# Kernel optimization log

Measured on AMD Instinct MI355X. Metric: run time of the kernel, lower is better.

Reference implementation:

```python
import jax, jax.numpy as jnp
import numpy as np

B, S, D, H = 2, 2048, 1024, 16
DK = D // H
NEG = -1.0e9

def setup_inputs() -> dict:
    key = jax.random.key(0)
    ks = jax.random.split(key, 12)
    sc = 1.0 / np.sqrt(D)
    q = jax.random.normal(ks[0], (B, S, D), jnp.float32)
    k = jax.random.normal(ks[1], (B, S, D), jnp.float32)
    v = jax.random.normal(ks[2], (B, S, D), jnp.float32)
    # causal mask: True = masked (matches masked_fill(mask == True, -1e9))
    mask = jnp.broadcast_to(jnp.triu(jnp.ones((S, S), bool), k=1)[None, None], (B, 1, S, S))
    Wq = jax.random.normal(ks[3], (D, D), jnp.float32) * sc
    bq = jnp.zeros((D,), jnp.float32)
    Wk = jax.random.normal(ks[4], (D, D), jnp.float32) * sc
    bk = jnp.zeros((D,), jnp.float32)
    Wv = jax.random.normal(ks[5], (D, D), jnp.float32) * sc
    bv = jnp.zeros((D,), jnp.float32)
    Wo = jax.random.normal(ks[6], (D, D), jnp.float32) * sc
    bo = jnp.zeros((D,), jnp.float32)
    return {"q": q, "k": k, "v": v, "mask": mask,
            "Wq": Wq, "bq": bq, "Wk": Wk, "bk": bk,
            "Wv": Wv, "bv": bv, "Wo": Wo, "bo": bo}

def reference(q, k, v, mask, Wq, bq, Wk, bk, Wv, bv, Wo, bo):
    def split_heads(x):  # [B,S,D] -> [B,H,S,DK]
        return x.reshape(B, S, H, DK).transpose(0, 2, 1, 3)
    qh = split_heads(q @ Wq + bq)
    kh = split_heads(k @ Wk + bk)
    vh = split_heads(v @ Wv + bv)
    scores = jnp.einsum('bhqd,bhkd->bhqk', qh, kh) / np.sqrt(DK)
    scores = jnp.where(mask, NEG, scores)
    p = jax.nn.softmax(scores, axis=-1)
    out = jnp.einsum('bhqk,bhkd->bhqd', p, vh)  # [B,H,S,DK]
    out = out.transpose(0, 2, 1, 3).reshape(B, S, D)
    return out @ Wo + bo
```

## Files before the change

kernel.cpp:

```cpp
#include <hip/hip_runtime.h>

#define BB 2
#define SS 2048
#define DD 1024
#define HH 16
#define DKK 64

typedef __attribute__((ext_vector_type(8))) short short8;
typedef __attribute__((ext_vector_type(4))) float floatx4;

__device__ inline float bf2f(ushort u) {
    union { unsigned int i; float f; } x; x.i = ((unsigned int)u) << 16; return x.f;
}
__device__ inline ushort f2bf(float f) {
    union { float f; unsigned int i; } x; x.f = f;
    unsigned int r = x.i + 0x7fff + ((x.i >> 16) & 1);
    return (ushort)(r >> 16);
}
__device__ inline void async_cp16(const ushort* g, ushort* l) {
    __builtin_amdgcn_global_load_lds(
        (const __attribute__((address_space(1))) unsigned int*)g,
        (__attribute__((address_space(3))) unsigned int*)l, 16, 0, 0);
}
__device__ inline unsigned int cvt_pk_bf16(float lo, float hi) {
    unsigned int r;
    asm("v_cvt_pk_bf16_f32 %0, %1, %2" : "=v"(r) : "v"(lo), "v"(hi));
    return r;
}
__device__ inline void swap32(unsigned int& a, unsigned int& b) {
    asm("v_permlane32_swap_b32 %0, %1" : "+v"(a), "+v"(b));
}
__device__ inline void swap16(unsigned int& a, unsigned int& b) {
    asm("v_permlane16_swap_b32 %0, %1" : "+v"(a), "+v"(b));
}

__global__ __launch_bounds__(256) void cvt_all(const float* __restrict__ q,
                                               const float* __restrict__ k,
                                               const float* __restrict__ v,
                                               const float* __restrict__ w0,
                                               const float* __restrict__ w1,
                                               const float* __restrict__ w2,
                                               const float* __restrict__ w3,
                                               ushort* __restrict__ oq,
                                               ushort* __restrict__ ok,
                                               ushort* __restrict__ ov,
                                               ushort* __restrict__ t0,
                                               ushort* __restrict__ t1,
                                               ushort* __restrict__ t2,
                                               ushort* __restrict__ t3) {
    __shared__ ushort t[32][33];
    int z = blockIdx.z;
    if (z < 3) {
        const float* in = (z == 0) ? q : (z == 1) ? k : v;
        ushort* out = (z == 0) ? oq : (z == 1) ? ok : ov;
        int i = blockIdx.x * 256 + threadIdx.x;
        float4 f0 = ((const float4*)in)[i * 2];
        float4 f1 = ((const float4*)in)[i * 2 + 1];
        short8 p;
        p[0] = (short)f2bf(f0.x); p[1] = (short)f2bf(f0.y);
        p[2] = (short)f2bf(f0.z); p[3] = (short)f2bf(f0.w);
        p[4] = (short)f2bf(f1.x); p[5] = (short)f2bf(f1.y);
        p[6] = (short)f2bf(f1.z); p[7] = (short)f2bf(f1.w);
        ((short8*)out)[i] = p;
    } else {
        int m = (z - 3) * 2 + (blockIdx.x >> 10);
        int tile = blockIdx.x & 1023;
        int bx = tile & 31, by = tile >> 5;
        const float* in = (m == 0) ? w0 : (m == 1) ? w1 : (m == 2) ? w2 : w3;
        ushort* out = (m == 0) ? t0 : (m == 1) ? t1 : (m == 2) ? t2 : t3;
        int tx = threadIdx.x & 31, ty = threadIdx.x >> 5;
        for (int i = ty; i < 32; i += 8)
            t[i][tx] = f2bf(in[(size_t)(by * 32 + i) * DD + bx * 32 + tx]);
        __syncthreads();
        for (int i = ty; i < 32; i += 8)
            out[(size_t)(bx * 32 + i) * DD + by * 32 + tx] = t[tx][i];
    }
}

__global__ __launch_bounds__(256, 3) void gemm_qkv(const ushort* __restrict__ Xq,
                                                   const ushort* __restrict__ Xk,
                                                   const ushort* __restrict__ Xv,
                                                   const ushort* __restrict__ WtQ,
                                                   const ushort* __restrict__ WtK,
                                                   const ushort* __restrict__ WtV,
                                                   const float* __restrict__ bq,
                                                   const float* __restrict__ bk,
                                                   const float* __restrict__ bv,
                                                   ushort* __restrict__ qh,
                                                   ushort* __restrict__ kh,
                                                   ushort* __restrict__ vt) {
    constexpr int K = 1024;
    constexpr int NKT = 32;
    __shared__ ushort smem[16384];

    int lin = blockIdx.x + ((blockIdx.y + (blockIdx.z << 5)) << 3);
    int wid = (lin & 7) * 96 + (lin >> 3);
    int z = wid >> 8;
    int rem = wid & 255;
    int byy = rem >> 3, bxx = rem & 7;
    int rowBase = byy * 128, colBase = bxx * 128;

    const ushort* Ag = (z == 0) ? Xq : (z == 1) ? Xk : Xv;
    const ushort* Bg = (z == 0) ? WtQ : (z == 1) ? WtK : WtV;
    const float* bias = (z == 0) ? bq : (z == 1) ? bk : bv;
    ushort* outp = (z == 0) ? qh : (z == 1) ? kh : vt;

    int tid = threadIdx.x;
    int wave = tid >> 6, lane = tid & 63, quad = lane >> 4, l15 = lane & 15;
    int wm = wave >> 1, wn = wave & 1;

    size_t srcA[2], srcB[2];
    int dstU[2];
#pragma unroll
    for (int r = 0; r < 2; ++r) {
        int lb = r * 4096 + wave * 1024 + lane * 16;
        int sl = lb ^ (((lb >> 9) & 1) << 5);
        int srow = sl >> 6;
        int scol = (sl & 63) >> 1;
        srcA[r] = (size_t)(rowBase + srow) * K + scol;
        srcB[r] = (size_t)(colBase + srow) * K + scol;
        dstU[r] = r * 2048 + wave * 512;
    }
    int aOff[4], bOff[4];
#pragma unroll
    for (int mi = 0; mi < 4; ++mi) {
        int row = wm * 64 + mi * 16 + l15;
        aOff[mi] = row * 32 + ((quad * 8) ^ (((row >> 3) & 1) << 4));
    }
#pragma unroll
    for (int ni = 0; ni < 4; ++ni) {
        int row = wn * 64 + ni * 16 + l15;
        bOff[ni] = 4096 + row * 32 + ((quad * 8) ^ (((row >> 3) & 1) << 4));
    }

    auto stageTile = [&](int u) {
        int slot = (u & 1) << 13;
        const ushort* As = Ag + u * 32;
        const ushort* Bs = Bg + u * 32;
        async_cp16(As + srcA[0], &smem[slot + dstU[0]]);
        async_cp16(As + srcA[1], &smem[slot + dstU[1]]);
        async_cp16(Bs + srcB[0], &smem[slot + 4096 + dstU[0]]);
        async_cp16(Bs + srcB[1], &smem[slot + 4096 + dstU[1]]);
    };

    floatx4 acc[4][4] = {};
    stageTile(0);
    for (int t = 0; t < NKT; ++t) {
        if (t < NKT - 1) {
            stageTile(t + 1);
            asm volatile("s_waitcnt vmcnt(4)" ::: "memory");
        } else {
            asm volatile("s_waitcnt vmcnt(0)" ::: "memory");
        }
        __builtin_amdgcn_s_barrier();
        __builtin_amdgcn_sched_barrier(0);
        int slot = (t & 1) << 13;
        short8 bfr[4], af[4];
#pragma unroll
        for (int ni = 0; ni < 4; ++ni)
            bfr[ni] = *(const short8*)&smem[slot + bOff[ni]];
#pragma unroll
        for (int mi = 0; mi < 4; ++mi)
            af[mi] = *(const short8*)&smem[slot + aOff[mi]];
#pragma unroll
        for (int mi = 0; mi < 4; ++mi)
#pragma unroll
            for (int ni = 0; ni < 4; ++ni)
                acc[mi][ni] = __builtin_amdgcn_mfma_f32_16x16x32_bf16(
                    af[mi], bfr[ni], acc[mi][ni], 0, 0, 0);
        __builtin_amdgcn_sched_barrier(0);
        __builtin_amdgcn_s_barrier();
    }

    float bvv[4];
#pragma unroll
    for (int ni = 0; ni < 4; ++ni)
        bvv[ni] = bias[colBase + wn * 64 + ni * 16 + l15];
    if (z == 2) {
#pragma unroll
        for (int mi = 0; mi < 4; ++mi)
#pragma unroll
            for (int ni = 0; ni < 4; ++ni) {
                int col = colBase + wn * 64 + ni * 16 + l15;
                int h = col >> 6, dk = col & 63;
                int rowg = rowBase + wm * 64 + mi * 16 + quad * 4;
                int b = rowg >> 11, s = rowg & 2047;
                int2 v;
                v.x = (int)cvt_pk_bf16(acc[mi][ni][0] + bvv[ni], acc[mi][ni][1] + bvv[ni]);
                v.y = (int)cvt_pk_bf16(acc[mi][ni][2] + bvv[ni], acc[mi][ni][3] + bvv[ni]);
                *(int2*)&outp[((size_t)((b * HH + h) * DKK + dk)) * SS + s] = v;
            }
    } else {
#pragma unroll
        for (int mi = 0; mi < 4; ++mi)
#pragma unroll
            for (int ni = 0; ni < 4; ++ni) {
                int col = colBase + wn * 64 + ni * 16 + l15;
                int h = col >> 6, dk = col & 63;
#pragma unroll
                for (int i = 0; i < 4; ++i) {
                    int rowg = rowBase + wm * 64 + mi * 16 + quad * 4 + i;
                    int b = rowg >> 11, s = rowg & 2047;
                    outp[((size_t)((b * HH + h) * SS + s)) * DKK + dk] =
                        f2bf(acc[mi][ni][i] + bvv[ni]);
                }
            }
    }
}

__global__ __launch_bounds__(256) void gemm_fin(const ushort* __restrict__ A,
                                                const ushort* __restrict__ Bt,
                                                const float* __restrict__ bias,
                                                float* __restrict__ outp) {
    constexpr int K = 1024, N = 1024, NT = 32;
    __shared__ ushort smem[12288];
    int tid = threadIdx.x;
    int wave = tid >> 6, lane = tid & 63, quad = lane >> 4, l15 = lane & 15;
    int wm = wave >> 1, wn = wave & 1;

    int lin = blockIdx.x + (blockIdx.y << 3);
    int wid = (lin & 7) * 64 + (lin >> 3);
    int bx = wid & 7, by = wid >> 3;
    int rowBase = by * 64, colBase = bx * 128;

    auto stage = [&](int k0, int d) {
        int ab = d * 6144, bb2 = 2048 + d * 6144;
#pragma unroll
        for (int j = 0; j < 3; ++j) {
            int c = j * 4 + wave;
            int cbase = (c < 4) ? c * 64 : (c - 4) * 64;
            int cc = cbase + lane;
            int row = cc >> 2, sub = (cc & 3) * 8;
            if (c < 4)
                async_cp16(&A[(size_t)(rowBase + row) * K + k0 + sub], &smem[ab + cbase * 8]);
            else
                async_cp16(&Bt[(size_t)(colBase + row) * K + k0 + sub], &smem[bb2 + cbase * 8]);
        }
    };

    floatx4 acc[2][4] = {};
    stage(0, 0);
    __syncthreads();
    for (int t = 0; t < NT; ++t) {
        if (t + 1 < NT) stage((t + 1) * 32, (t + 1) & 1);
        int ab = (t & 1) * 6144, bb2 = 2048 + (t & 1) * 6144;
        short8 af[2], bf[4];
#pragma unroll
        for (int mi = 0; mi < 2; ++mi)
            af[mi] = *(const short8*)&smem[ab + (wm * 32 + mi * 16 + l15) * 32 + quad * 8];
#pragma unroll
        for (int ni = 0; ni < 4; ++ni)
            bf[ni] = *(const short8*)&smem[bb2 + (wn * 64 + ni * 16 + l15) * 32 + quad * 8];
#pragma unroll
        for (int mi = 0; mi < 2; ++mi)
#pragma unroll
            for (int ni = 0; ni < 4; ++ni)
                acc[mi][ni] = __builtin_amdgcn_mfma_f32_16x16x32_bf16(
                    af[mi], bf[ni], acc[mi][ni], 0, 0, 0);
        __syncthreads();
    }
    for (int mi = 0; mi < 2; ++mi)
        for (int ni = 0; ni < 4; ++ni) {
            int col = colBase + wn * 64 + ni * 16 + l15;
            float bv = bias[col];
            for (int i = 0; i < 4; ++i) {
                int row = rowBase + wm * 32 + mi * 16 + quad * 4 + i;
                outp[(size_t)row * N + col] = acc[mi][ni][i] + bv;
            }
        }
}

__global__ __launch_bounds__(256, 2) void flash_attn5(const ushort* __restrict__ qh,
                                                      const ushort* __restrict__ kh,
                                                      const ushort* __restrict__ vt,
                                                      ushort* __restrict__ attn) {
    constexpr int LD = 72;
    __shared__ ushort Ksm[2][64 * LD];
    __shared__ ushort Vsm[2][64 * LD];
    int tid = threadIdx.x;
    int wave = tid >> 6, lane = tid & 63, quad = lane >> 4, l15 = lane & 15;

    int lin = blockIdx.x + (blockIdx.y << 4) + (blockIdx.z << 8);
    int wid = (lin & 7) * 64 + (lin >> 3);
    const int qt0 = wid & 15;
    int h = (wid >> 4) & 15;
    int b = wid >> 8;
    const int qt1 = 31 - qt0;

    const size_t headQK = ((size_t)(b * HH + h)) * SS * DKK;
    const size_t headV  = ((size_t)(b * HH + h)) * DKK * SS;
    int c0 = tid, r0 = c0 >> 3, s0 = (c0 & 7) * 8;
    int c1 = tid + 256, r1 = c1 >> 3, s1 = (c1 & 7) * 8;

    int qrow0 = qt0 * 64 + wave * 16 + l15;
    int qrow1 = qt1 * 64 + wave * 16 + l15;
    short8 q0a = *(const short8*)&qh[headQK + (size_t)qrow0 * DKK + quad * 8];
    short8 q0b = *(const short8*)&qh[headQK + (size_t)qrow0 * DKK + 32 + quad * 8];
    short8 q1a = *(const short8*)&qh[headQK + (size_t)qrow1 * DKK + quad * 8];
    short8 q1b = *(const short8*)&qh[headQK + (size_t)qrow1 * DKK + 32 + quad * 8];

    floatx4 o0[4] = {}, o1[4] = {};
    float l0 = 0.f, l1 = 0.f;
    int qsel = wave * 16 + l15;

    *(int4*)&Ksm[0][r0 * LD + s0] = *(const int4*)&kh[headQK + (size_t)r0 * DKK + s0];
    *(int4*)&Ksm[0][r1 * LD + s1] = *(const int4*)&kh[headQK + (size_t)r1 * DKK + s1];
    *(int4*)&Vsm[0][r0 * LD + s0] = *(const int4*)&vt[headV + (size_t)r0 * SS + s0];
    *(int4*)&Vsm[0][r1 * LD + s1] = *(const int4*)&vt[headV + (size_t)r1 * SS + s1];
    __syncthreads();

    for (int kt = 0; kt <= qt1; ++kt) {
        int cur = kt & 1;
        bool pre = (kt < qt1);
        bool act0 = (kt <= qt0);
        int4 kA, kB, vA, vB;
        if (pre) {
            const ushort* kp = &kh[headQK + (size_t)((kt + 1) * 64) * DKK];
            const ushort* vp = &vt[headV + (kt + 1) * 64];
            kA = *(const int4*)&kp[(size_t)r0 * DKK + s0];
            kB = *(const int4*)&kp[(size_t)r1 * DKK + s1];
            vA = *(const int4*)&vp[(size_t)r0 * SS + s0];
            vB = *(const int4*)&vp[(size_t)r1 * SS + s1];
        }
        floatx4 sv1[4], sv0[4];
        __builtin_amdgcn_s_setprio(1);
#pragma unroll
        for (int cn = 0; cn < 4; ++cn) {
            short8 kf0 = *(const short8*)&Ksm[cur][(cn * 16 + l15) * LD + quad * 8];
            short8 kf1 = *(const short8*)&Ksm[cur][(cn * 16 + l15) * LD + 32 + quad * 8];
            floatx4 zz = {};
            zz = __builtin_amdgcn_mfma_f32_16x16x32_bf16(kf0, q1a, zz, 0, 0, 0);
            zz = __builtin_amdgcn_mfma_f32_16x16x32_bf16(kf1, q1b, zz, 0, 0, 0);
            sv1[cn] = zz;
            if (act0) {
                floatx4 y = {};
                y = __builtin_amdgcn_mfma_f32_16x16x32_bf16(kf0, q0a, y, 0, 0, 0);
                y = __builtin_amdgcn_mfma_f32_16x16x32_bf16(kf1, q0b, y, 0, 0, 0);
                sv0[cn] = y;
            }
        }
        __builtin_amdgcn_s_setprio(0);
        short8 vf[2][4];
#pragma unroll
        for (int ks = 0; ks < 2; ++ks)
#pragma unroll
            for (int n = 0; n < 4; ++n)
                vf[ks][n] = *(const short8*)&Vsm[cur][(n * 16 + l15) * LD + ks * 32 + quad * 8];

        {
            bool diag = (kt == qt1);
            unsigned int pkd[4][2];
#pragma unroll
            for (int cn = 0; cn < 4; ++cn) {
#pragma unroll
                for (int i = 0; i < 4; ++i) {
                    float p = __expf(sv1[cn][i] * 0.125f);
                    if (diag && (cn * 16 + quad * 4 + i) > qsel) p = 0.f;
                    sv1[cn][i] = p;
                    l1 += p;
                }
                pkd[cn][0] = cvt_pk_bf16(sv1[cn][0], sv1[cn][1]);
                pkd[cn][1] = cvt_pk_bf16(sv1[cn][2], sv1[cn][3]);
            }
            __builtin_amdgcn_s_setprio(1);
#pragma unroll
            for (int ks = 0; ks < 2; ++ks) {
                unsigned int a0 = pkd[ks * 2][0], b0 = pkd[ks * 2 + 1][0];
                swap32(a0, b0); swap16(a0, b0);
                unsigned int a1 = pkd[ks * 2][1], b1 = pkd[ks * 2 + 1][1];
                swap32(a1, b1); swap16(a1, b1);
                union { int4 i4; short8 s8; } u;
                u.i4 = make_int4((int)a0, (int)a1, (int)b0, (int)b1);
#pragma unroll
                for (int n = 0; n < 4; ++n)
                    o1[n] = __builtin_amdgcn_mfma_f32_16x16x32_bf16(
                        vf[ks][n], u.s8, o1[n], 0, 0, 0);
            }
            __builtin_amdgcn_s_setprio(0);
        }
        if (act0) {
            bool diag = (kt == qt0);
            unsigned int pkd[4][2];
#pragma unroll
            for (int cn = 0; cn < 4; ++cn) {
#pragma unroll
                for (int i = 0; i < 4; ++i) {
                    float p = __expf(sv0[cn][i] * 0.125f);
                    if (diag && (cn * 16 + quad * 4 + i) > qsel) p = 0.f;
                    sv0[cn][i] = p;
                    l0 += p;
                }
                pkd[cn][0] = cvt_pk_bf16(sv0[cn][0], sv0[cn][1]);
                pkd[cn][1] = cvt_pk_bf16(sv0[cn][2], sv0[cn][3]);
            }
            __builtin_amdgcn_s_setprio(1);
#pragma unroll
            for (int ks = 0; ks < 2; ++ks) {
                unsigned int a0 = pkd[ks * 2][0], b0 = pkd[ks * 2 + 1][0];
                swap32(a0, b0); swap16(a0, b0);
                unsigned int a1 = pkd[ks * 2][1], b1 = pkd[ks * 2 + 1][1];
                swap32(a1, b1); swap16(a1, b1);
                union { int4 i4; short8 s8; } u;
                u.i4 = make_int4((int)a0, (int)a1, (int)b0, (int)b1);
#pragma unroll
                for (int n = 0; n < 4; ++n)
                    o0[n] = __builtin_amdgcn_mfma_f32_16x16x32_bf16(
                        vf[ks][n], u.s8, o0[n], 0, 0, 0);
            }
            __builtin_amdgcn_s_setprio(0);
        }
        if (pre) {
            int nb = cur ^ 1;
            *(int4*)&Ksm[nb][r0 * LD + s0] = kA;
            *(int4*)&Ksm[nb][r1 * LD + s1] = kB;
            *(int4*)&Vsm[nb][r0 * LD + s0] = vA;
            *(int4*)&Vsm[nb][r1 * LD + s1] = vB;
        }
        __syncthreads();
    }
    l0 += __shfl_xor(l0, 16, 64); l0 += __shfl_xor(l0, 32, 64);
    l1 += __shfl_xor(l1, 16, 64); l1 += __shfl_xor(l1, 32, 64);
    float inv0 = 1.0f / l0, inv1 = 1.0f / l1;
    size_t rowOff0 = ((size_t)(b * SS + qt0 * 64 + wave * 16 + l15)) * DD + h * 64;
    size_t rowOff1 = ((size_t)(b * SS + qt1 * 64 + wave * 16 + l15)) * DD + h * 64;
#pragma unroll
    for (int n = 0; n < 4; ++n) {
        int dof = n * 16 + quad * 4;
        int2 v0, v1;
        v0.x = (int)cvt_pk_bf16(o0[n][0] * inv0, o0[n][1] * inv0);
        v0.y = (int)cvt_pk_bf16(o0[n][2] * inv0, o0[n][3] * inv0);
        v1.x = (int)cvt_pk_bf16(o1[n][0] * inv1, o1[n][1] * inv1);
        v1.y = (int)cvt_pk_bf16(o1[n][2] * inv1, o1[n][3] * inv1);
        *(int2*)&attn[rowOff0 + dof] = v0;
        *(int2*)&attn[rowOff1 + dof] = v1;
    }
}

extern "C" void kernel_launch(void* const* d_in, const int* in_sizes, int n_in,
                              void* d_out, int out_size, void* d_ws, size_t ws_size,
                              hipStream_t stream) {
    const float* q  = (const float*)d_in[0];
    const float* k  = (const float*)d_in[1];
    const float* v  = (const float*)d_in[2];
    const float* Wq = (const float*)d_in[4];
    const float* bq = (const float*)d_in[5];
    const float* Wk = (const float*)d_in[6];
    const float* bk = (const float*)d_in[7];
    const float* Wv = (const float*)d_in[8];
    const float* bv = (const float*)d_in[9];
    const float* Wo = (const float*)d_in[10];
    const float* bo = (const float*)d_in[11];

    ushort* ws   = (ushort*)d_ws;
    ushort* WtQ  = ws;
    ushort* WtK  = WtQ + (1u << 20);
    ushort* WtV  = WtK + (1u << 20);
    ushort* WtO  = WtV + (1u << 20);
    ushort* Xv   = WtO + (1u << 20);
    ushort* qh   = Xv + (4u << 20);
    ushort* kh   = qh + (4u << 20);
    ushort* vt   = kh + (4u << 20);
    ushort* Xq   = (ushort*)d_out;
    ushort* Xk   = Xq + (4u << 20);
    ushort* attn = Xv;

    cvt_all<<<dim3(2048, 1, 5), 256, 0, stream>>>(q, k, v, Wq, Wk, Wv, Wo,
                                                  Xq, Xk, Xv,
                                                  WtQ, WtK, WtV, WtO);

    gemm_qkv<<<dim3(8, 32, 3), 256, 0, stream>>>(Xq, Xk, Xv, WtQ, WtK, WtV,
                                                 bq, bk, bv, qh, kh, vt);

    flash_attn5<<<dim3(16, 16, 2), 256, 0, stream>>>(qh, kh, vt, attn);

    gemm_fin<<<dim3(8, 64), 256, 0, stream>>>(attn, WtO, bo, (float*)d_out);
}
```

Baseline: 228.5 us.

## Split flash attention over key range with combine kernel; swizzle gemm_fin LDS pipeline

```diff
diff --git a/kernel.cpp b/kernel.cpp
--- a/kernel.cpp
+++ b/kernel.cpp
@@ -208,11 +208,11 @@
     }
 }
 
-__global__ __launch_bounds__(256) void gemm_fin(const ushort* __restrict__ A,
-                                                const ushort* __restrict__ Bt,
-                                                const float* __restrict__ bias,
-                                                float* __restrict__ outp) {
-    constexpr int K = 1024, N = 1024, NT = 32;
+__global__ __launch_bounds__(256, 2) void gemm_fin(const ushort* __restrict__ A,
+                                                   const ushort* __restrict__ Bt,
+                                                   const float* __restrict__ bias,
+                                                   float* __restrict__ outp) {
+    constexpr int K = 1024, N = 1024, NKT = 32;
     __shared__ ushort smem[12288];
     int tid = threadIdx.x;
     int wave = tid >> 6, lane = tid & 63, quad = lane >> 4, l15 = lane & 15;
@@ -223,41 +223,69 @@
     int bx = wid & 7, by = wid >> 3;
     int rowBase = by * 64, colBase = bx * 128;
 
-    auto stage = [&](int k0, int d) {
-        int ab = d * 6144, bb2 = 2048 + d * 6144;
-#pragma unroll
-        for (int j = 0; j < 3; ++j) {
-            int c = j * 4 + wave;
-            int cbase = (c < 4) ? c * 64 : (c - 4) * 64;
-            int cc = cbase + lane;
-            int row = cc >> 2, sub = (cc & 3) * 8;
-            if (c < 4)
-                async_cp16(&A[(size_t)(rowBase + row) * K + k0 + sub], &smem[ab + cbase * 8]);
-            else
-                async_cp16(&Bt[(size_t)(colBase + row) * K + k0 + sub], &smem[bb2 + cbase * 8]);
-        }
+    size_t srcA; int dstA;
+    {
+        int lb = wave * 1024 + lane * 16;
+        int sl = lb ^ (((lb >> 9) & 1) << 5);
+        srcA = (size_t)(rowBase + (sl >> 6)) * K + ((sl & 63) >> 1);
+        dstA = wave * 512;
+    }
+    size_t srcB[2]; int dstB[2];
+#pragma unroll
+    for (int r = 0; r < 2; ++r) {
+        int lb = r * 4096 + wave * 1024 + lane * 16;
+        int sl = lb ^ (((lb >> 9) & 1) << 5);
+        srcB[r] = (size_t)(colBase + (sl >> 6)) * K + ((sl & 63) >> 1);
+        dstB[r] = 2048 + r * 2048 + wave * 512;
+    }
+    int aOff[2], bOff[4];
+#pragma unroll
+    for (int mi = 0; mi < 2; ++mi) {
+        int row = wm * 32 + mi * 16 + l15;
+        aOff[mi] = row * 32 + ((quad * 8) ^ (((row >> 3) & 1) << 4));
+    }
+#pragma unroll
+    for (int ni = 0; ni < 4; ++ni) {
+        int row = wn * 64 + ni * 16 + l15;
+        bOff[ni] = 2048 + row * 32 + ((quad * 8) ^ (((row >> 3) & 1) << 4));
+    }
+
+    auto stageTile = [&](int u) {
+        int slot = (u & 1) * 6144;
+        const ushort* As = A + u * 32;
+        const ushort* Bs = Bt + u * 32;
+        async_cp16(As + srcA, &smem[slot + dstA]);
+        async_cp16(Bs + srcB[0], &smem[slot + dstB[0]]);
+        async_cp16(Bs + srcB[1], &smem[slot + dstB[1]]);
     };
 
     floatx4 acc[2][4] = {};
-    stage(0, 0);
-    __syncthreads();
-    for (int t = 0; t < NT; ++t) {
-        if (t + 1 < NT) stage((t + 1) * 32, (t + 1) & 1);
-        int ab = (t & 1) * 6144, bb2 = 2048 + (t & 1) * 6144;
-        short8 af[2], bf[4];
+    stageTile(0);
+    for (int t = 0; t < NKT; ++t) {
+        if (t < NKT - 1) {
+            stageTile(t + 1);
+            asm volatile("s_waitcnt vmcnt(3)" ::: "memory");
+        } else {
+            asm volatile("s_waitcnt vmcnt(0)" ::: "memory");
+        }
+        __builtin_amdgcn_s_barrier();
+        __builtin_amdgcn_sched_barrier(0);
+        int slot = (t & 1) * 6144;
+        short8 af[2], bfr[4];
+#pragma unroll
+        for (int ni = 0; ni < 4; ++ni)
+            bfr[ni] = *(const short8*)&smem[slot + bOff[ni]];
 #pragma unroll
         for (int mi = 0; mi < 2; ++mi)
-            af[mi] = *(const short8*)&smem[ab + (wm * 32 + mi * 16 + l15) * 32 + quad * 8];
-#pragma unroll
-        for (int ni = 0; ni < 4; ++ni)
-            bf[ni] = *(const short8*)&smem[bb2 + (wn * 64 + ni * 16 + l15) * 32 + quad * 8];
+            af[mi] = *(const short8*)&smem[slot + aOff[mi]];
 #pragma unroll
         for (int mi = 0; mi < 2; ++mi)
 #pragma unroll
             for (int ni = 0; ni < 4; ++ni)
                 acc[mi][ni] = __builtin_amdgcn_mfma_f32_16x16x32_bf16(
-                    af[mi], bf[ni], acc[mi][ni], 0, 0, 0);
-        __syncthreads();
+                    af[mi], bfr[ni], acc[mi][ni], 0, 0, 0);
+        __builtin_amdgcn_sched_barrier(0);
+        __builtin_amdgcn_s_barrier();
     }
     for (int mi = 0; mi < 2; ++mi)
         for (int ni = 0; ni < 4; ++ni) {
@@ -270,22 +298,31 @@
         }
 }
 
-__global__ __launch_bounds__(256, 2) void flash_attn5(const ushort* __restrict__ qh,
+__global__ __launch_bounds__(256, 4) void flash_split(const ushort* __restrict__ qh,
                                                       const ushort* __restrict__ kh,
                                                       const ushort* __restrict__ vt,
-                                                      ushort* __restrict__ attn) {
+                                                      float* __restrict__ oP0,
+                                                      float* __restrict__ oP1,
+                                                      float* __restrict__ lP0,
+                                                      float* __restrict__ lP1) {
     constexpr int LD = 72;
     __shared__ ushort Ksm[2][64 * LD];
     __shared__ ushort Vsm[2][64 * LD];
     int tid = threadIdx.x;
     int wave = tid >> 6, lane = tid & 63, quad = lane >> 4, l15 = lane & 15;
 
-    int lin = blockIdx.x + (blockIdx.y << 4) + (blockIdx.z << 8);
-    int wid = (lin & 7) * 64 + (lin >> 3);
-    const int qt0 = wid & 15;
-    int h = (wid >> 4) & 15;
-    int b = wid >> 8;
+    int lin = blockIdx.x + (blockIdx.y << 5) + (blockIdx.z << 9);
+    int wid = (lin & 7) * 128 + (lin >> 3);
+    int half = wid & 1;
+    const int qt0 = (wid >> 1) & 15;
+    int h = (wid >> 5) & 15;
+    int b = wid >> 9;
     const int qt1 = 31 - qt0;
+    int mid = (qt1 + 1) >> 1;
+    int k0 = half ? mid : 0;
+    int k1 = half ? qt1 : mid - 1;
+    float* oP = half ? oP1 : oP0;
+    float* lP = half ? lP1 : lP0;
 
     const size_t headQK = ((size_t)(b * HH + h)) * SS * DKK;
     const size_t headV  = ((size_t)(b * HH + h)) * DKK * SS;
@@ -303,15 +340,19 @@
     float l0 = 0.f, l1 = 0.f;
     int qsel = wave * 16 + l15;
 
-    *(int4*)&Ksm[0][r0 * LD + s0] = *(const int4*)&kh[headQK + (size_t)r0 * DKK + s0];
-    *(int4*)&Ksm[0][r1 * LD + s1] = *(const int4*)&kh[headQK + (size_t)r1 * DKK + s1];
-    *(int4*)&Vsm[0][r0 * LD + s0] = *(const int4*)&vt[headV + (size_t)r0 * SS + s0];
-    *(int4*)&Vsm[0][r1 * LD + s1] = *(const int4*)&vt[headV + (size_t)r1 * SS + s1];
+    {
+        const ushort* kp = &kh[headQK + (size_t)(k0 * 64) * DKK];
+        const ushort* vp = &vt[headV + k0 * 64];
+        *(int4*)&Ksm[0][r0 * LD + s0] = *(const int4*)&kp[(size_t)r0 * DKK + s0];
+        *(int4*)&Ksm[0][r1 * LD + s1] = *(const int4*)&kp[(size_t)r1 * DKK + s1];
+        *(int4*)&Vsm[0][r0 * LD + s0] = *(const int4*)&vp[(size_t)r0 * SS + s0];
+        *(int4*)&Vsm[0][r1 * LD + s1] = *(const int4*)&vp[(size_t)r1 * SS + s1];
+    }
     __syncthreads();
 
-    for (int kt = 0; kt <= qt1; ++kt) {
-        int cur = kt & 1;
-        bool pre = (kt < qt1);
+    for (int kt = k0; kt <= k1; ++kt) {
+        int cur = (kt - k0) & 1;
+        bool pre = (kt < k1);
         bool act0 = (kt <= qt0);
         int4 kA, kB, vA, vB;
         if (pre) {
@@ -420,20 +461,70 @@
     }
     l0 += __shfl_xor(l0, 16, 64); l0 += __shfl_xor(l0, 32, 64);
     l1 += __shfl_xor(l1, 16, 64); l1 += __shfl_xor(l1, 32, 64);
-    float inv0 = 1.0f / l0, inv1 = 1.0f / l1;
-    size_t rowOff0 = ((size_t)(b * SS + qt0 * 64 + wave * 16 + l15)) * DD + h * 64;
-    size_t rowOff1 = ((size_t)(b * SS + qt1 * 64 + wave * 16 + l15)) * DD + h * 64;
-#pragma unroll
-    for (int n = 0; n < 4; ++n) {
-        int dof = n * 16 + quad * 4;
-        int2 v0, v1;
-        v0.x = (int)cvt_pk_bf16(o0[n][0] * inv0, o0[n][1] * inv0);
-        v0.y = (int)cvt_pk_bf16(o0[n][2] * inv0, o0[n][3] * inv0);
-        v1.x = (int)cvt_pk_bf16(o1[n][0] * inv1, o1[n][1] * inv1);
-        v1.y = (int)cvt_pk_bf16(o1[n][2] * inv1, o1[n][3] * inv1);
-        *(int2*)&attn[rowOff0 + dof] = v0;
-        *(int2*)&attn[rowOff1 + dof] = v1;
-    }
+    size_t lBase = ((size_t)(b * HH + h)) * SS;
+    if (quad == 0) {
+        lP[lBase + qt0 * 64 + wave * 16 + l15] = l0;
+        lP[lBase + qt1 * 64 + wave * 16 + l15] = l1;
+    }
+    float* fbuf = (float*)&Ksm[0][0];
+#pragma unroll
+    for (int n = 0; n < 4; ++n)
+#pragma unroll
+        for (int i = 0; i < 4; ++i)
+            fbuf[(wave * 16 + l15) * 64 + n * 16 + quad * 4 + i] = o0[n][i];
+    __syncthreads();
+    {
+        size_t base = (lBase + qt0 * 64) * 64;
+#pragma unroll
+        for (int u = 0; u < 4; ++u) {
+            int idx = u * 256 + tid;
+            ((float4*)&oP[base])[idx] = ((const float4*)fbuf)[idx];
+        }
+    }
+    __syncthreads();
+#pragma unroll
+    for (int n = 0; n < 4; ++n)
+#pragma unroll
+        for (int i = 0; i < 4; ++i)
+            fbuf[(wave * 16 + l15) * 64 + n * 16 + quad * 4 + i] = o1[n][i];
+    __syncthreads();
+    {
+        size_t base = (lBase + qt1 * 64) * 64;
+#pragma unroll
+        for (int u = 0; u < 4; ++u) {
+            int idx = u * 256 + tid;
+            ((float4*)&oP[base])[idx] = ((const float4*)fbuf)[idx];
+        }
+    }
+}
+
+__global__ __launch_bounds__(256) void combine_attn(const float* __restrict__ oP0,
+                                                    const float* __restrict__ oP1,
+                                                    const float* __restrict__ lP0,
+                                                    const float* __restrict__ lP1,
+                                                    ushort* __restrict__ attn) {
+    int t = blockIdx.x * 256 + threadIdx.x;
+    int bhq = t >> 2;
+    int seg = t & 3;
+    int b = bhq >> 15, h = (bhq >> 11) & 15, qq = bhq & 2047;
+    float inv = 1.0f / (lP0[bhq] + lP1[bhq]);
+    size_t src = (size_t)bhq * 64 + seg * 16;
+    float4 a0 = ((const float4*)&oP0[src])[0], b0 = ((const float4*)&oP1[src])[0];
+    float4 a1 = ((const float4*)&oP0[src])[1], b1 = ((const float4*)&oP1[src])[1];
+    float4 a2 = ((const float4*)&oP0[src])[2], b2 = ((const float4*)&oP1[src])[2];
+    float4 a3 = ((const float4*)&oP0[src])[3], b3 = ((const float4*)&oP1[src])[3];
+    int4 w0, w1;
+    w0.x = (int)cvt_pk_bf16((a0.x + b0.x) * inv, (a0.y + b0.y) * inv);
+    w0.y = (int)cvt_pk_bf16((a0.z + b0.z) * inv, (a0.w + b0.w) * inv);
+    w0.z = (int)cvt_pk_bf16((a1.x + b1.x) * inv, (a1.y + b1.y) * inv);
+    w0.w = (int)cvt_pk_bf16((a1.z + b1.z) * inv, (a1.w + b1.w) * inv);
+    w1.x = (int)cvt_pk_bf16((a2.x + b2.x) * inv, (a2.y + b2.y) * inv);
+    w1.y = (int)cvt_pk_bf16((a2.z + b2.z) * inv, (a2.w + b2.w) * inv);
+    w1.z = (int)cvt_pk_bf16((a3.x + b3.x) * inv, (a3.y + b3.y) * inv);
+    w1.w = (int)cvt_pk_bf16((a3.z + b3.z) * inv, (a3.w + b3.w) * inv);
+    size_t dst = ((size_t)(b * SS + qq)) * DD + h * 64 + seg * 16;
+    *(int4*)&attn[dst] = w0;
+    *(int4*)&attn[dst + 8] = w1;
 }
 
 extern "C" void kernel_launch(void* const* d_in, const int* in_sizes, int n_in,
@@ -456,22 +547,28 @@
     ushort* WtK  = WtQ + (1u << 20);
     ushort* WtV  = WtK + (1u << 20);
     ushort* WtO  = WtV + (1u << 20);
-    ushort* Xv   = WtO + (1u << 20);
-    ushort* qh   = Xv + (4u << 20);
+    ushort* attn = WtO + (1u << 20);
+    ushort* qh   = attn + (4u << 20);
     ushort* kh   = qh + (4u << 20);
     ushort* vt   = kh + (4u << 20);
+    float*  oP1  = (float*)(ws + (20u << 20));
+    float*  lP0  = (float*)(ws + (28u << 20));
+    float*  lP1  = lP0 + (BB * HH * SS);
     ushort* Xq   = (ushort*)d_out;
     ushort* Xk   = Xq + (4u << 20);
-    ushort* attn = Xv;
+    float*  oP0  = (float*)d_out;
 
     cvt_all<<<dim3(2048, 1, 5), 256, 0, stream>>>(q, k, v, Wq, Wk, Wv, Wo,
-                                                  Xq, Xk, Xv,
+                                                  Xq, Xk, attn,
                                                   WtQ, WtK, WtV, WtO);
 
-    gemm_qkv<<<dim3(8, 32, 3), 256, 0, stream>>>(Xq, Xk, Xv, WtQ, WtK, WtV,
+    gemm_qkv<<<dim3(8, 32, 3), 256, 0, stream>>>(Xq, Xk, attn, WtQ, WtK, WtV,
                                                  bq, bk, bv, qh, kh, vt);
 
-    flash_attn5<<<dim3(16, 16, 2), 256, 0, stream>>>(qh, kh, vt, attn);
+    flash_split<<<dim3(32, 16, 2), 256, 0, stream>>>(qh, kh, vt,
+                                                     oP0, oP1, lP0, lP1);
+
+    combine_attn<<<dim3(1024), 256, 0, stream>>>(oP0, oP1, lP0, lP1, attn);
 
     gemm_fin<<<dim3(8, 64), 256, 0, stream>>>(attn, WtO, bo, (float*)d_out);
 }
```

Result: slower. 288.2 us (+26.1%).
